# Optimization experiments

Measured on AMD Instinct MI355X. Metric: run time of the kernel, lower is better.

Reference implementation:

```python
import jax, jax.numpy as jnp
import numpy as np

EPS = 1e-3


def setup_inputs() -> dict:
    key = jax.random.key(0)
    k1, k2, k3, k4 = jax.random.split(key, 4)
    B, D, F = 1024, 1024, 32768
    x = jax.random.normal(k1, (B, D), jnp.float32)
    y = jax.random.normal(k2, (B, D), jnp.float32)
    xs = jax.random.normal(k3, (F, D), jnp.float32)
    xs = xs / jnp.linalg.norm(xs, axis=-1, keepdims=True)  # step() stores unit-norm atoms
    ys = jax.random.normal(k4, (F, D), jnp.float32)
    ys = ys / jnp.linalg.norm(ys, axis=-1, keepdims=True)
    return {"x": x, "y": y, "xs": xs, "ys": ys, "target_l0": 32}


def _grad_pursuit(signal, dictionary, target_l0):
    # signal: [B, V]; dictionary: [F, V]
    B = signal.shape[0]
    F = dictionary.shape[0]
    rows = jnp.arange(B)

    def step(weights, _):
        residual = signal - jnp.einsum('bf,fv->bv', weights, dictionary)  # [B, V]
        inner_products = jnp.einsum('bv,fv->bf', residual, dictionary)    # [B, F]
        idx = jnp.argmax(inner_products, axis=1)                          # [B]
        selected = (weights != 0).at[rows, idx].set(True)                 # [B, F] bool
        grad = jnp.where(selected, inner_products, jnp.zeros((), signal.dtype))
        c = jnp.einsum('bf,fv->bv', grad, dictionary)                     # [B, V]
        c_sq = jnp.sum(c * c, axis=-1)
        step_size = jnp.sum(c * residual, axis=-1) / jnp.maximum(c_sq, EPS)
        weights = jax.nn.relu(weights + step_size[:, None] * grad)
        return weights, None

    weights0 = jnp.zeros((B, F), signal.dtype)
    weights, _ = jax.lax.scan(step, weights0, None, length=target_l0)
    return jax.lax.top_k(weights, target_l0)  # (values [B,k], indices [B,k])


def _decode(indices, weights, dictionary):
    # embedding-bag sum: gather [B,k,V] atoms, weight, sum over k
    return jnp.einsum('bk,bkv->bv', weights, dictionary[indices])


def reference(x, y, xs, ys, target_l0):
    weights, indices = _grad_pursuit(x, xs, target_l0)
    x_reconstructed = _decode(indices, weights, xs)
    y_reconstructed = _decode(indices, weights, ys)
    losses = jnp.sum((y_reconstructed - y) ** 2, axis=-1)
    return weights, indices, x_reconstructed, y_reconstructed, losses
```

## Files before the change

### kernel.cpp

```cpp
#include <hip/hip_runtime.h>

#define B_ 1024
#define D_ 1024
#define F_ 32768
#define T_ 32
#define KSLOTS 32

#define LO_SCALE     2048.0f
#define LO_INV_SCALE 4.8828125e-4f

typedef _Float16 f16x8 __attribute__((ext_vector_type(8)));
typedef _Float16 f16x4 __attribute__((ext_vector_type(4)));
typedef float    f32x4 __attribute__((ext_vector_type(4)));

__device__ __forceinline__ unsigned int fkey(float f) {
    unsigned int u = __float_as_uint(f);
    return (u & 0x80000000u) ? ~u : (u | 0x80000000u);
}
__device__ __forceinline__ unsigned long long packkey(float v, unsigned int n) {
    return ((unsigned long long)fkey(v) << 32) | (unsigned long long)(0xFFFFFFFFu - n);
}

__device__ __forceinline__ void async16(const void* g, void* l) {
    __builtin_amdgcn_global_load_lds(
        (const __attribute__((address_space(1))) unsigned int*)g,
        (__attribute__((address_space(3))) unsigned int*)l, 16, 0, 0);
}

__device__ __forceinline__ f32x4 mfma16(f16x8 a, f16x8 b, f32x4 c) {
    return __builtin_amdgcn_mfma_f32_16x16x32_f16(a, b, c, 0, 0, 0);
}

__device__ __forceinline__ void fsplit(float v, _Float16& h, _Float16& l) {
    h = (_Float16)v;
    l = (_Float16)((v - (float)h) * LO_SCALE);
}

__global__ __launch_bounds__(256) void split_xs_kernel(
    const float* __restrict__ XS, _Float16* __restrict__ hi, _Float16* __restrict__ lo)
{
    const size_t i = ((size_t)blockIdx.x * 256 + threadIdx.x) * 4;
    const float4 v = *(const float4*)(XS + i);
    f16x4 hv, lv;
    _Float16 h, l;
    fsplit(v.x, h, l); hv[0] = h; lv[0] = l;
    fsplit(v.y, h, l); hv[1] = h; lv[1] = l;
    fsplit(v.z, h, l); hv[2] = h; lv[2] = l;
    fsplit(v.w, h, l); hv[3] = h; lv[3] = l;
    *(f16x4*)(hi + i) = hv;
    *(f16x4*)(lo + i) = lv;
}

__global__ __launch_bounds__(256) void init_kernel(
    const float* __restrict__ X, float* __restrict__ Rres,
    _Float16* __restrict__ Rhi, _Float16* __restrict__ Rlo,
    int* __restrict__ a_cnt, unsigned long long* __restrict__ amax)
{
    const int b = blockIdx.x, tid = threadIdx.x;
    for (int d = tid; d < D_; d += 256) {
        const float v = X[(size_t)b * D_ + d];
        Rres[(size_t)b * D_ + d] = v;
        _Float16 h, l; fsplit(v, h, l);
        Rhi[(size_t)b * D_ + d] = h;
        Rlo[(size_t)b * D_ + d] = l;
    }
    if (tid == 0) { a_cnt[b] = 0; amax[b] = 0ull; }
}

#define SPL1(H, L, I, V) { _Float16 _h; _Float16 _l; fsplit((V), _h, _l); H[I] = _h; L[I] = _l; }

#define WAIT_VM8()  { asm volatile("s_waitcnt vmcnt(8)" ::: "memory"); }
#define WAIT_VM0()  { asm volatile("s_waitcnt vmcnt(0)" ::: "memory"); }
#define BARRIER_PIN() { __builtin_amdgcn_s_barrier(); __builtin_amdgcn_sched_barrier(0); }

template <bool PRE>
__global__ __launch_bounds__(256, 2) void gemm16_argmax_kernel(
    const _Float16* __restrict__ Ahi, const _Float16* __restrict__ Alo,
    const _Float16* __restrict__ Bhi, const _Float16* __restrict__ Blo,
    const float* __restrict__ XSf,
    unsigned long long* __restrict__ amax)
{
    __shared__ __align__(16) _Float16 As[2][2][128][32];
    __shared__ __align__(16) _Float16 Bs[2][2][128][32];
    __shared__ unsigned long long red[128][2];

    const int tid  = threadIdx.x;
    const int wid  = tid >> 6, lane = tid & 63;
    const int orig = (int)blockIdx.x;
    const int wgid = (orig & 7) * 256 + (orig >> 3);
    const int m0   = (wgid & 7) * 128;
    const int n0   = (wgid >> 3) * 128;
    const int wm   = wid >> 1, wn = wid & 1;

    f32x4 acc[4][4], acc2[4][4];
#pragma unroll
    for (int i = 0; i < 4; ++i)
#pragma unroll
        for (int j = 0; j < 4; ++j) {
            acc[i][j]  = (f32x4){0.f, 0.f, 0.f, 0.f};
            acc2[i][j] = (f32x4){0.f, 0.f, 0.f, 0.f};
        }

    const int srow = wid * 32 + (lane >> 2);
    const int skof = (lane & 3) * 8;
    const _Float16* gAh = Ahi + (size_t)(m0 + srow) * D_ + skof;
    const _Float16* gAl = Alo + (size_t)(m0 + srow) * D_ + skof;
    const _Float16* gBh = nullptr;
    const _Float16* gBl = nullptr;
    const float*    gBf = nullptr;
    if constexpr (PRE) {
        gBh = Bhi + (size_t)(n0 + srow) * D_ + skof;
        gBl = Blo + (size_t)(n0 + srow) * D_ + skof;
    } else {
        gBf = XSf + (size_t)(n0 + (tid >> 1)) * D_ + (tid & 1) * 16;
    }

    const int lrow = lane & 15;
    const int lk   = (lane >> 4) * 8;

    auto stageAB = [&](int bb, int k0) {
#pragma unroll
        for (int c = 0; c < 2; ++c) {
            const size_t go = (size_t)(c * 16) * D_ + k0;
            const int    ro = wid * 32 + c * 16;
            async16(gAh + go, &As[bb][0][ro][0]);
            async16(gAl + go, &As[bb][1][ro][0]);
            async16(gBh + go, &Bs[bb][0][ro][0]);
            async16(gBl + go, &Bs[bb][1][ro][0]);
        }
    };
    auto stageA = [&](int bb, int k0) {
#pragma unroll
        for (int c = 0; c < 2; ++c) {
            const size_t go = (size_t)(c * 16) * D_ + k0;
            const int    ro = wid * 32 + c * 16;
            async16(gAh + go, &As[bb][0][ro][0]);
            async16(gAl + go, &As[bb][1][ro][0]);
        }
    };
    float4 q0, q1, q2, q3;
    auto loadB = [&](int k0) {
        q0 = *(const float4*)(gBf + k0);
        q1 = *(const float4*)(gBf + k0 + 4);
        q2 = *(const float4*)(gBf + k0 + 8);
        q3 = *(const float4*)(gBf + k0 + 12);
    };
    auto writeB = [&](int bb) {
        const int br = tid >> 1, bq = (tid & 1) * 16;
        f16x8 h0, l0, h1, l1;
        SPL1(h0, l0, 0, q0.x) SPL1(h0, l0, 1, q0.y) SPL1(h0, l0, 2, q0.z) SPL1(h0, l0, 3, q0.w)
        SPL1(h0, l0, 4, q1.x) SPL1(h0, l0, 5, q1.y) SPL1(h0, l0, 6, q1.z) SPL1(h0, l0, 7, q1.w)
        SPL1(h1, l1, 0, q2.x) SPL1(h1, l1, 1, q2.y) SPL1(h1, l1, 2, q2.z) SPL1(h1, l1, 3, q2.w)
        SPL1(h1, l1, 4, q3.x) SPL1(h1, l1, 5, q3.y) SPL1(h1, l1, 6, q3.z) SPL1(h1, l1, 7, q3.w)
        *(f16x8*)&Bs[bb][0][br][bq]     = h0;
        *(f16x8*)&Bs[bb][0][br][bq + 8] = h1;
        *(f16x8*)&Bs[bb][1][br][bq]     = l0;
        *(f16x8*)&Bs[bb][1][br][bq + 8] = l1;
    };
    auto compute = [&](int bb) {
        f16x8 ah[4], al[4], bh[4], bl[4];
#pragma unroll
        for (int i = 0; i < 4; ++i) {
            ah[i] = *(const f16x8*)&As[bb][0][wm * 64 + i * 16 + lrow][lk];
            al[i] = *(const f16x8*)&As[bb][1][wm * 64 + i * 16 + lrow][lk];
            bh[i] = *(const f16x8*)&Bs[bb][0][wn * 64 + i * 16 + lrow][lk];
            bl[i] = *(const f16x8*)&Bs[bb][1][wn * 64 + i * 16 + lrow][lk];
        }
#pragma unroll
        for (int i = 0; i < 4; ++i)
#pragma unroll
            for (int j = 0; j < 4; ++j) {
                acc[i][j]  = mfma16(ah[i], bh[j], acc[i][j]);
                acc2[i][j] = mfma16(ah[i], bl[j], acc2[i][j]);
                acc2[i][j] = mfma16(al[i], bh[j], acc2[i][j]);
            }
    };

    if constexpr (PRE) {
        stageAB(0, 0);
        WAIT_VM0();
        BARRIER_PIN();
        for (int k0 = 0; k0 < D_; k0 += 64) {
            if (k0 + 32 < D_) { stageAB(1, k0 + 32); WAIT_VM8(); }
            else              { WAIT_VM0(); }
            BARRIER_PIN();
            compute(0);
            BARRIER_PIN();
            if (k0 + 64 < D_) { stageAB(0, k0 + 64); WAIT_VM8(); }
            else              { WAIT_VM0(); }
            BARRIER_PIN();
            compute(1);
            BARRIER_PIN();
        }
    } else {
        loadB(0); stageA(0, 0); writeB(0);
        __syncthreads();
        for (int k0 = 0; k0 < D_; k0 += 64) {
            if (k0 + 32 < D_) { loadB(k0 + 32); stageA(1, k0 + 32); }
            compute(0);
            if (k0 + 32 < D_) writeB(1);
            __syncthreads();
            if (k0 + 64 < D_) { loadB(k0 + 64); stageA(0, k0 + 64); }
            compute(1);
            if (k0 + 64 < D_) writeB(0);
            __syncthreads();
        }
    }

    const unsigned cb = (unsigned)(n0 + wn * 64 + (lane & 15));
#pragma unroll
    for (int mi = 0; mi < 4; ++mi) {
#pragma unroll
        for (int r = 0; r < 4; ++r) {
            unsigned long long best = 0ull;
#pragma unroll
            for (int j = 0; j < 4; ++j) {
                const float v = acc[mi][j][r] + acc2[mi][j][r] * LO_INV_SCALE;
                const unsigned long long key = packkey(v, cb + (unsigned)(j * 16));
                best = key > best ? key : best;
            }
#pragma unroll
            for (int off = 1; off < 16; off <<= 1) {
                const unsigned long long o = __shfl_xor(best, off);
                best = o > best ? o : best;
            }
            if ((lane & 15) == 0)
                red[wm * 64 + mi * 16 + ((lane >> 4) << 2) + r][wn] = best;
        }
    }
    __syncthreads();
    if (tid < 128) {
        const unsigned long long b0 = red[tid][0], b1 = red[tid][1];
        atomicMax(&amax[m0 + tid], b0 > b1 ? b0 : b1);
    }
}

__global__ __launch_bounds__(256) void update_kernel(
    const float* __restrict__ X, const float* __restrict__ XS,
    float* __restrict__ Rres,
    _Float16* __restrict__ Rhi, _Float16* __restrict__ Rlo,
    int* __restrict__ a_idx, float* __restrict__ a_w, int* __restrict__ a_cnt,
    unsigned long long* __restrict__ amax)
{
    const int b = blockIdx.x;
    const int tid = threadIdx.x;
    __shared__ float s_r[D_];
    __shared__ int   s_idx[33];
    __shared__ float s_w[33];
    __shared__ float s_g[33];
    __shared__ int   s_cnt;
    __shared__ float s_red[8];

    for (int d = tid; d < D_; d += 256) s_r[d] = Rres[(size_t)b * D_ + d];

    if (tid == 0) {
        int cnt = a_cnt[b];
        for (int j = 0; j < cnt; ++j) { s_idx[j] = a_idx[b*KSLOTS + j]; s_w[j] = a_w[b*KSLOTS + j]; }
        unsigned long long key = amax[b];
        int ni = (int)(0xFFFFFFFFu - (unsigned int)(key & 0xFFFFFFFFull));
        bool found = false;
        for (int j = 0; j < cnt; ++j) found = found || (s_idx[j] == ni);
        if (!found) {
            int p = cnt;
            while (p > 0 && s_idx[p-1] > ni) { s_idx[p] = s_idx[p-1]; s_w[p] = s_w[p-1]; --p; }
            s_idx[p] = ni; s_w[p] = 0.f; ++cnt;
        }
        s_cnt = cnt;
    }
    __syncthreads();
    const int cnt = s_cnt;
    const int wave = tid >> 6, lane = tid & 63;

    for (int j = wave; j < cnt; j += 4) {
        const float* xr = XS + (size_t)s_idx[j] * D_;
        float sum = 0.f;
#pragma unroll
        for (int i = 0; i < D_/64; ++i) { int d = lane + (i << 6); sum = fmaf(s_r[d], xr[d], sum); }
        for (int off = 32; off > 0; off >>= 1) sum += __shfl_down(sum, off);
        if (lane == 0) s_g[j] = sum;
    }
    __syncthreads();

    float cs = 0.f, cr = 0.f;
#pragma unroll
    for (int v = 0; v < 4; ++v) {
        const int d = tid + (v << 8);
        float cv = 0.f;
        for (int j = 0; j < cnt; ++j) cv = fmaf(s_g[j], XS[(size_t)s_idx[j]*D_ + d], cv);
        cs = fmaf(cv, cv, cs);
        cr = fmaf(cv, s_r[d], cr);
    }
    for (int off = 32; off > 0; off >>= 1) { cs += __shfl_down(cs, off); cr += __shfl_down(cr, off); }
    if (lane == 0) { s_red[wave] = cs; s_red[4 + wave] = cr; }
    __syncthreads();

    if (tid == 0) {
        const float cs_t = s_red[0] + s_red[1] + s_red[2] + s_red[3];
        const float cr_t = s_red[4] + s_red[5] + s_red[6] + s_red[7];
        const float ss = cr_t / fmaxf(cs_t, 1e-3f);
        int nc = 0;
        for (int j = 0; j < cnt; ++j) {
            float nw = s_w[j] + ss * s_g[j];
            if (nw > 0.f) { s_idx[nc] = s_idx[j]; s_w[nc] = nw; ++nc; }
        }
        s_cnt = nc;
        a_cnt[b] = nc;
        for (int j = 0; j < nc; ++j) { a_idx[b*KSLOTS + j] = s_idx[j]; a_w[b*KSLOTS + j] = s_w[j]; }
        amax[b] = 0ull;
    }
    __syncthreads();
    const int nc = s_cnt;

#pragma unroll
    for (int v = 0; v < 4; ++v) {
        const int d = tid + (v << 8);
        float s = 0.f;
        for (int j = 0; j < nc; ++j) s = fmaf(s_w[j], XS[(size_t)s_idx[j]*D_ + d], s);
        const float rv = X[(size_t)b*D_ + d] - s;
        Rres[(size_t)b*D_ + d] = rv;
        _Float16 h, l; fsplit(rv, h, l);
        Rhi[(size_t)b*D_ + d] = h;
        Rlo[(size_t)b*D_ + d] = l;
    }
}

__global__ __launch_bounds__(256) void finalize_kernel(
    const float* __restrict__ Y,
    const float* __restrict__ XS, const float* __restrict__ YS,
    const int* __restrict__ a_idx, const float* __restrict__ a_w, const int* __restrict__ a_cnt,
    float* __restrict__ out)
{
    const int b = blockIdx.x, tid = threadIdx.x;
    __shared__ int   s_idx[KSLOTS];
    __shared__ float s_w[KSLOTS];
    __shared__ int   o_idx[KSLOTS];
    __shared__ float o_w[KSLOTS];
    __shared__ float s_red[4];

    if (tid == 0) {
        int cnt = a_cnt[b];
        for (int j = 0; j < cnt; ++j) { s_idx[j] = a_idx[b*KSLOTS + j]; s_w[j] = a_w[b*KSLOTS + j]; }
        for (int i = 1; i < cnt; ++i) {
            int ii = s_idx[i]; float ww = s_w[i];
            int p = i - 1;
            while (p >= 0 && (s_w[p] < ww || (s_w[p] == ww && s_idx[p] > ii))) {
                s_w[p+1] = s_w[p]; s_idx[p+1] = s_idx[p]; --p;
            }
            s_w[p+1] = ww; s_idx[p+1] = ii;
        }
        for (int j = 0; j < cnt; ++j) { o_idx[j] = s_idx[j]; o_w[j] = s_w[j]; }
        int p = cnt, f = 0;
        while (p < KSLOTS) {
            bool member = false;
            for (int j = 0; j < cnt; ++j) member = member || (s_idx[j] == f);
            if (!member) { o_idx[p] = f; o_w[p] = 0.f; ++p; }
            ++f;
        }
    }
    __syncthreads();

    if (tid < KSLOTS) {
        out[(size_t)b*KSLOTS + tid] = o_w[tid];
        out[32768 + (size_t)b*KSLOTS + tid] = (float)o_idx[tid];
    }

    float lsum = 0.f;
    for (int d = tid; d < D_; d += 256) {
        float xr = 0.f, yr = 0.f;
#pragma unroll
        for (int k = 0; k < KSLOTS; ++k) {
            const size_t off = (size_t)o_idx[k] * D_ + d;
            xr = fmaf(o_w[k], XS[off], xr);
            yr = fmaf(o_w[k], YS[off], yr);
        }
        out[65536 + (size_t)b*D_ + d] = xr;
        out[65536 + 1048576 + (size_t)b*D_ + d] = yr;
        const float e = yr - Y[(size_t)b*D_ + d];
        lsum = fmaf(e, e, lsum);
    }
    const int wave = tid >> 6, lane = tid & 63;
    for (int off = 32; off > 0; off >>= 1) lsum += __shfl_down(lsum, off);
    if (lane == 0) s_red[wave] = lsum;
    __syncthreads();
    if (tid == 0) out[65536 + 2097152 + b] = s_red[0] + s_red[1] + s_red[2] + s_red[3];
}

extern "C" void kernel_launch(void* const* d_in, const int* in_sizes, int n_in,
                              void* d_out, int out_size, void* d_ws, size_t ws_size,
                              hipStream_t stream) {
    (void)in_sizes; (void)n_in; (void)out_size;
    const float* x  = (const float*)d_in[0];
    const float* y  = (const float*)d_in[1];
    const float* xs = (const float*)d_in[2];
    const float* ys = (const float*)d_in[3];
    float* out = (float*)d_out;

    char* ws = (char*)d_ws;
    float*              Rres  = (float*)(ws);
    _Float16*           Rhi   = (_Float16*)(ws + ((size_t)4 << 20));
    _Float16*           Rlo   = (_Float16*)(ws + ((size_t)6 << 20));
    unsigned long long* amax  = (unsigned long long*)(ws + ((size_t)8 << 20));
    int*                a_cnt = (int*)(ws + ((size_t)8 << 20) + 8192);
    int*                a_idx = (int*)(ws + ((size_t)8 << 20) + 8192 + 4096);
    float*              a_w   = (float*)(ws + ((size_t)8 << 20) + 8192 + 4096 + 131072);
    _Float16*           XShi  = (_Float16*)(ws + ((size_t)16 << 20));
    _Float16*           XSlo  = (_Float16*)(ws + ((size_t)80 << 20));
    const bool big = ws_size >= ((size_t)144 << 20);

    if (big) split_xs_kernel<<<(F_ * D_) / 1024, 256, 0, stream>>>(xs, XShi, XSlo);
    init_kernel<<<B_, 256, 0, stream>>>(x, Rres, Rhi, Rlo, a_cnt, amax);

    for (int t = 0; t < T_; ++t) {
        if (big)
            gemm16_argmax_kernel<true ><<<dim3(2048), 256, 0, stream>>>(Rhi, Rlo, XShi, XSlo, xs, amax);
        else
            gemm16_argmax_kernel<false><<<dim3(2048), 256, 0, stream>>>(Rhi, Rlo, nullptr, nullptr, xs, amax);
        update_kernel<<<B_, 256, 0, stream>>>(x, xs, Rres, Rhi, Rlo, a_idx, a_w, a_cnt, amax);
    }
    finalize_kernel<<<B_, 256, 0, stream>>>(y, xs, ys, a_idx, a_w, a_cnt, out);
}
```

Before: 8.231 ms.

## Switch split-fp16 GEMM to 32x32x16 MFMA with swizzled LDS layout

Replaces the 16x16x32 MFMA tiling in the GEMM+argmax kernel with 32x32x16 MFMA instructions, so each wave holds 2x2 32x32 accumulators. It also applies an XOR-style rotation swizzle to the k-chunk offsets in both the async global->LDS staging and the register-side B writes, to avoid LDS bank conflicts on the new read pattern. The epilogue argmax is reworked for the 32x32 output layout, using a 32-lane shuffle reduction. Larger MFMAs reduce LDS read traffic and instruction count per FLOP, at the cost of reworked index maps that must stay consistent across staging, reads and epilogue.

```diff
diff --git a/kernel.cpp b/kernel.cpp
--- a/kernel.cpp
+++ b/kernel.cpp
@@ -9,9 +9,9 @@
 #define LO_SCALE     2048.0f
 #define LO_INV_SCALE 4.8828125e-4f
 
-typedef _Float16 f16x8 __attribute__((ext_vector_type(8)));
-typedef _Float16 f16x4 __attribute__((ext_vector_type(4)));
-typedef float    f32x4 __attribute__((ext_vector_type(4)));
+typedef _Float16 f16x8  __attribute__((ext_vector_type(8)));
+typedef _Float16 f16x4  __attribute__((ext_vector_type(4)));
+typedef float    f32x16 __attribute__((ext_vector_type(16)));
 
 __device__ __forceinline__ unsigned int fkey(float f) {
     unsigned int u = __float_as_uint(f);
@@ -27,8 +27,8 @@
         (__attribute__((address_space(3))) unsigned int*)l, 16, 0, 0);
 }
 
-__device__ __forceinline__ f32x4 mfma16(f16x8 a, f16x8 b, f32x4 c) {
-    return __builtin_amdgcn_mfma_f32_16x16x32_f16(a, b, c, 0, 0, 0);
+__device__ __forceinline__ f32x16 mfma32(f16x8 a, f16x8 b, f32x16 c) {
+    return __builtin_amdgcn_mfma_f32_32x32x16_f16(a, b, c, 0, 0, 0);
 }
 
 __device__ __forceinline__ void fsplit(float v, _Float16& h, _Float16& l) {
@@ -92,17 +92,17 @@
     const int n0   = (wgid >> 3) * 128;
     const int wm   = wid >> 1, wn = wid & 1;
 
-    f32x4 acc[4][4], acc2[4][4];
-#pragma unroll
-    for (int i = 0; i < 4; ++i)
-#pragma unroll
-        for (int j = 0; j < 4; ++j) {
-            acc[i][j]  = (f32x4){0.f, 0.f, 0.f, 0.f};
-            acc2[i][j] = (f32x4){0.f, 0.f, 0.f, 0.f};
+    f32x16 acc[2][2], acc2[2][2];
+#pragma unroll
+    for (int i = 0; i < 2; ++i)
+#pragma unroll
+        for (int j = 0; j < 2; ++j) {
+#pragma unroll
+            for (int t = 0; t < 16; ++t) { acc[i][j][t] = 0.f; acc2[i][j][t] = 0.f; }
         }
 
     const int srow = wid * 32 + (lane >> 2);
-    const int skof = (lane & 3) * 8;
+    const int skof = 8 * (((lane & 3) - ((lane >> 2) & 3)) & 3);
     const _Float16* gAh = Ahi + (size_t)(m0 + srow) * D_ + skof;
     const _Float16* gAl = Alo + (size_t)(m0 + srow) * D_ + skof;
     const _Float16* gBh = nullptr;
@@ -115,8 +115,9 @@
         gBf = XSf + (size_t)(n0 + (tid >> 1)) * D_ + (tid & 1) * 16;
     }
 
-    const int lrow = lane & 15;
-    const int lk   = (lane >> 4) * 8;
+    const int lrow = lane & 31;
+    const int qsw0 = 8 * ((0 + (lane >> 5) + (lane & 3)) & 3);
+    const int qsw1 = 8 * ((2 + (lane >> 5) + (lane & 3)) & 3);
 
     auto stageAB = [&](int bb, int k0) {
 #pragma unroll
@@ -146,34 +147,45 @@
         q3 = *(const float4*)(gBf + k0 + 12);
     };
     auto writeB = [&](int bb) {
-        const int br = tid >> 1, bq = (tid & 1) * 16;
+        const int br = tid >> 1;
+        const int u  = (tid & 1) * 2;
+        const int p0 = 8 * (((u + 0) + (br & 3)) & 3);
+        const int p1 = 8 * (((u + 1) + (br & 3)) & 3);
         f16x8 h0, l0, h1, l1;
         SPL1(h0, l0, 0, q0.x) SPL1(h0, l0, 1, q0.y) SPL1(h0, l0, 2, q0.z) SPL1(h0, l0, 3, q0.w)
         SPL1(h0, l0, 4, q1.x) SPL1(h0, l0, 5, q1.y) SPL1(h0, l0, 6, q1.z) SPL1(h0, l0, 7, q1.w)
         SPL1(h1, l1, 0, q2.x) SPL1(h1, l1, 1, q2.y) SPL1(h1, l1, 2, q2.z) SPL1(h1, l1, 3, q2.w)
         SPL1(h1, l1, 4, q3.x) SPL1(h1, l1, 5, q3.y) SPL1(h1, l1, 6, q3.z) SPL1(h1, l1, 7, q3.w)
-        *(f16x8*)&Bs[bb][0][br][bq]     = h0;
-        *(f16x8*)&Bs[bb][0][br][bq + 8] = h1;
-        *(f16x8*)&Bs[bb][1][br][bq]     = l0;
-        *(f16x8*)&Bs[bb][1][br][bq + 8] = l1;
+        *(f16x8*)&Bs[bb][0][br][p0] = h0;
+        *(f16x8*)&Bs[bb][0][br][p1] = h1;
+        *(f16x8*)&Bs[bb][1][br][p0] = l0;
+        *(f16x8*)&Bs[bb][1][br][p1] = l1;
     };
     auto compute = [&](int bb) {
-        f16x8 ah[4], al[4], bh[4], bl[4];
-#pragma unroll
-        for (int i = 0; i < 4; ++i) {
-            ah[i] = *(const f16x8*)&As[bb][0][wm * 64 + i * 16 + lrow][lk];
-            al[i] = *(const f16x8*)&As[bb][1][wm * 64 + i * 16 + lrow][lk];
-            bh[i] = *(const f16x8*)&Bs[bb][0][wn * 64 + i * 16 + lrow][lk];
-            bl[i] = *(const f16x8*)&Bs[bb][1][wn * 64 + i * 16 + lrow][lk];
-        }
-#pragma unroll
-        for (int i = 0; i < 4; ++i)
-#pragma unroll
-            for (int j = 0; j < 4; ++j) {
-                acc[i][j]  = mfma16(ah[i], bh[j], acc[i][j]);
-                acc2[i][j] = mfma16(ah[i], bl[j], acc2[i][j]);
-                acc2[i][j] = mfma16(al[i], bh[j], acc2[i][j]);
-            }
+        f16x8 ah[2][2], al[2][2], bh[2][2], bl[2][2];
+#pragma unroll
+        for (int t = 0; t < 2; ++t) {
+            const int ra = wm * 64 + t * 32 + lrow;
+            const int rb = wn * 64 + t * 32 + lrow;
+            ah[t][0] = *(const f16x8*)&As[bb][0][ra][qsw0];
+            ah[t][1] = *(const f16x8*)&As[bb][0][ra][qsw1];
+            al[t][0] = *(const f16x8*)&As[bb][1][ra][qsw0];
+            al[t][1] = *(const f16x8*)&As[bb][1][ra][qsw1];
+            bh[t][0] = *(const f16x8*)&Bs[bb][0][rb][qsw0];
+            bh[t][1] = *(const f16x8*)&Bs[bb][0][rb][qsw1];
+            bl[t][0] = *(const f16x8*)&Bs[bb][1][rb][qsw0];
+            bl[t][1] = *(const f16x8*)&Bs[bb][1][rb][qsw1];
+        }
+#pragma unroll
+        for (int i = 0; i < 2; ++i)
+#pragma unroll
+            for (int j = 0; j < 2; ++j)
+#pragma unroll
+                for (int kh = 0; kh < 2; ++kh) {
+                    acc[i][j]  = mfma32(ah[i][kh], bh[j][kh], acc[i][j]);
+                    acc2[i][j] = mfma32(ah[i][kh], bl[j][kh], acc2[i][j]);
+                    acc2[i][j] = mfma32(al[i][kh], bh[j][kh], acc2[i][j]);
+                }
     };
 
     if constexpr (PRE) {
@@ -207,25 +219,25 @@
         }
     }
 
-    const unsigned cb = (unsigned)(n0 + wn * 64 + (lane & 15));
-#pragma unroll
-    for (int mi = 0; mi < 4; ++mi) {
-#pragma unroll
-        for (int r = 0; r < 4; ++r) {
-            unsigned long long best = 0ull;
-#pragma unroll
-            for (int j = 0; j < 4; ++j) {
-                const float v = acc[mi][j][r] + acc2[mi][j][r] * LO_INV_SCALE;
-                const unsigned long long key = packkey(v, cb + (unsigned)(j * 16));
-                best = key > best ? key : best;
-            }
-#pragma unroll
-            for (int off = 1; off < 16; off <<= 1) {
+    const unsigned cbase = (unsigned)(n0 + wn * 64 + (lane & 31));
+    const int rl4 = 4 * (lane >> 5);
+#pragma unroll
+    for (int mi = 0; mi < 2; ++mi) {
+#pragma unroll
+        for (int t = 0; t < 16; ++t) {
+            const int rloc = (t & 3) + 8 * (t >> 2) + rl4;
+            const float v0 = acc[mi][0][t] + acc2[mi][0][t] * LO_INV_SCALE;
+            const float v1 = acc[mi][1][t] + acc2[mi][1][t] * LO_INV_SCALE;
+            const unsigned long long k0 = packkey(v0, cbase);
+            const unsigned long long k1 = packkey(v1, cbase + 32u);
+            unsigned long long best = k0 > k1 ? k0 : k1;
+#pragma unroll
+            for (int off = 1; off < 32; off <<= 1) {
                 const unsigned long long o = __shfl_xor(best, off);
                 best = o > best ? o : best;
             }
-            if ((lane & 15) == 0)
-                red[wm * 64 + mi * 16 + ((lane >> 4) << 2) + r][wn] = best;
+            if ((lane & 31) == 0)
+                red[wm * 64 + mi * 32 + rloc][wn] = best;
         }
     }
     __syncthreads();
```

After: 9.930 ms. +20.6%, slower.
